# Kernel optimization log

Measured on AMD Instinct MI355X. Metric: run time of the kernel, lower is better.

## Reference

```python
import jax, jax.numpy as jnp
import numpy as np

N_NODES = 50000
N_EDGES = 800000
D_IN = 512
D_HID = 256


def gcn_conv(x, W, b, src, dst, n_nodes):
    """PyG-style GCNConv: self-loops + symmetric normalization.
    x: [N, d_in], W: [d_in, d_out], b: [d_out], src/dst: [E] (already include self-loops? no -> add here)
    """
    loops = jnp.arange(n_nodes, dtype=src.dtype)
    src_f = jnp.concatenate([src, loops])  # [E+N]
    dst_f = jnp.concatenate([dst, loops])
    deg = jax.ops.segment_sum(jnp.ones_like(dst_f, dtype=x.dtype), dst_f,
                              num_segments=n_nodes)  # [N]
    dinv = jnp.where(deg > 0, jax.lax.rsqrt(deg), 0.0)
    norm = dinv[src_f] * dinv[dst_f]  # [E+N]
    h = x @ W  # [N, d_out] -- dense GEMM
    msg = h[src_f] * norm[:, None]  # gather + scale, [E+N, d_out]
    out = jax.ops.segment_sum(msg, dst_f, num_segments=n_nodes)  # scatter-add
    return out + b


def setup_inputs() -> dict:
    key = jax.random.key(0)
    k1, k2, k3, k4, k5 = jax.random.split(key, 5)
    x = jax.random.normal(k1, (N_NODES, D_IN), dtype=jnp.float32)
    edge_index = jax.random.randint(k2, (2, N_EDGES), 0, N_NODES, dtype=jnp.int32)
    # Glorot-ish init for weights
    W1 = jax.random.normal(k3, (D_IN, D_HID), dtype=jnp.float32) / np.sqrt(D_IN)
    W2 = jax.random.normal(k4, (D_HID, D_HID), dtype=jnp.float32) / np.sqrt(D_HID)
    b1 = jnp.zeros((D_HID,), dtype=jnp.float32)
    b2 = jnp.zeros((D_HID,), dtype=jnp.float32)
    return {"x": x, "edge_index": edge_index, "W1": W1, "b1": b1, "W2": W2, "b2": b2}


def reference(x, edge_index, W1, b1, W2, b2):
    n_nodes = x.shape[0]
    src, dst = edge_index[0], edge_index[1]
    h = jax.nn.relu(gcn_conv(x, W1, b1, src, dst, n_nodes))
    h = gcn_conv(h, W2, b2, src, dst, n_nodes)
    # edge-level gather-dot scoring
    score = jnp.einsum('ed,ed->e', h[src], h[dst])  # [E]
    prob_edge = jax.nn.sigmoid(score)
    return prob_edge
```

## Files before the change

### kernel.cpp

```cpp
#include <hip/hip_runtime.h>
#include <stdint.h>

#define D_IN 512
#define D_HID 256

typedef __attribute__((ext_vector_type(8))) short bf16x8;
typedef __attribute__((ext_vector_type(8))) unsigned short u16x8;
typedef __attribute__((ext_vector_type(4))) float f32x4;

__device__ __forceinline__ float b2f(unsigned short u) {
    union { float f; uint32_t i; } x; x.i = ((uint32_t)u) << 16; return x.f;
}
__device__ __forceinline__ unsigned short f2b(float f) {
    union { float f; uint32_t i; } x; x.f = f;
    uint32_t i = x.i;
    uint32_t r = (i + 0x7FFFu + ((i >> 16) & 1u)) >> 16;
    return (unsigned short)r;
}

__device__ __forceinline__ void async_copy16(const unsigned short* g, unsigned short* lds) {
    __builtin_amdgcn_global_load_lds((const __attribute__((address_space(1))) unsigned int*)g,
                                     (__attribute__((address_space(3))) unsigned int*)lds,
                                     16, 0, 0);
}

__global__ __launch_bounds__(256) void detect_dtype_kernel(const ushort4* __restrict__ raw,
                                                           int n4, int* __restrict__ flag) {
    int i = blockIdx.x * blockDim.x + threadIdx.x;
    int hit = 0;
    if (i < n4) {
        ushort4 u = raw[i];
        hit = ((((u.x >> 7) & 0xFF) == 0xFF) || (((u.y >> 7) & 0xFF) == 0xFF) ||
               (((u.z >> 7) & 0xFF) == 0xFF) || (((u.w >> 7) & 0xFF) == 0xFF)) ? 1 : 0;
    }
    unsigned long long b = __ballot(hit);
    if ((threadIdx.x & 63) == 0 && b != 0ULL) atomicOr(flag, 1);
}

__device__ __forceinline__ void wpack_body(const void* __restrict__ W,
        unsigned short* __restrict__ Wp, int K, bool f32, int t) {
    int total = (K >> 6) * 2 * 16 * 64;
    if (t >= total) return;
    int lane = t & 63;
    int c = (t >> 6) & 15;
    int h = (t >> 10) & 1;
    int kk = t >> 11;
    int n = c * 16 + (lane & 15);
    int k0 = kk * 64 + h * 32 + (lane >> 4) * 8;
    u16x8 o;
#pragma unroll
    for (int j = 0; j < 8; ++j) {
        float v = f32 ? ((const float*)W)[(size_t)(k0 + j) * 256 + n]
                      : b2f(((const unsigned short*)W)[(size_t)(k0 + j) * 256 + n]);
        o[j] = f2b(v);
    }
    *(u16x8*)(Wp + (size_t)t * 8) = o;
}

__global__ __launch_bounds__(256) void pre_fused_kernel(const int* __restrict__ dst,
        int* __restrict__ counts, int E,
        const void* __restrict__ W1, unsigned short* __restrict__ Wp1,
        const void* __restrict__ W2, unsigned short* __restrict__ Wp2,
        const int* __restrict__ flag, int histBlocks, int wp1Blocks) {
    int b = blockIdx.x;
    if (b < histBlocks) {
        int e = b * 256 + threadIdx.x;
        if (e < E) atomicAdd(&counts[dst[e]], 1);
        return;
    }
    b -= histBlocks;
    bool f32 = (*flag != 0);
    if (b < wp1Blocks) {
        wpack_body(W1, Wp1, D_IN, f32, b * 256 + threadIdx.x);
    } else {
        wpack_body(W2, Wp2, D_HID, f32, (b - wp1Blocks) * 256 + threadIdx.x);
    }
}

__global__ __launch_bounds__(256) void partial_sum_kernel(const int* __restrict__ counts,
        int* __restrict__ partial, int n) {
    __shared__ int sh[4];
    int b = blockIdx.x;
    int lane = threadIdx.x & 63, wv = threadIdx.x >> 6;
    int s = 0;
    for (int j = threadIdx.x; j < 1024; j += 256) {
        int i = b * 1024 + j;
        s += (i < n) ? counts[i] : 0;
    }
#pragma unroll
    for (int off = 32; off > 0; off >>= 1) s += __shfl_down(s, off, 64);
    if (lane == 0) sh[wv] = s;
    __syncthreads();
    if (threadIdx.x == 0) partial[b] = sh[0] + sh[1] + sh[2] + sh[3];
}

__global__ void scan_partials_kernel(int* __restrict__ partial, int nb,
                                     int* __restrict__ indptr, int N) {
    int lane = threadIdx.x & 63;
    int orig = (lane < nb) ? partial[lane] : 0;
    int v = orig;
#pragma unroll
    for (int off = 1; off < 64; off <<= 1) {
        int u = __shfl(v, lane - off, 64);
        if (lane >= off) v += u;
    }
    int tot = __shfl(v, nb - 1, 64);
    if (lane < nb) partial[lane] = v - orig;
    if (lane == 0) indptr[N] = tot;
}

__global__ __launch_bounds__(1024) void scan_chunk_kernel(const int* __restrict__ counts,
        const int* __restrict__ partial, int* __restrict__ indptr, int* __restrict__ cursor,
        float* __restrict__ dinv, int n) {
    __shared__ int sh[1024];
    int b = blockIdx.x;
    int i = b * 1024 + threadIdx.x;
    int v = (i < n) ? counts[i] : 0;
    sh[threadIdx.x] = v;
    __syncthreads();
    for (int off = 1; off < 1024; off <<= 1) {
        int t = (threadIdx.x >= off) ? sh[threadIdx.x - off] : 0;
        __syncthreads();
        sh[threadIdx.x] += t;
        __syncthreads();
    }
    if (i < n) {
        int e = partial[b] + sh[threadIdx.x] - v;
        indptr[i] = e;
        cursor[i] = e;
        dinv[i] = rsqrtf((float)(v + 1));
    }
}

template<int K, bool MF32, bool FUSE>
__global__ __launch_bounds__(256) void gemm_bf16(const void* __restrict__ Ain,
        const unsigned short* __restrict__ Wp, unsigned short* __restrict__ C, int M,
        const int* __restrict__ flag,
        const int* __restrict__ eidx, int* __restrict__ cursor, int* __restrict__ csr_src,
        int* __restrict__ csr_dst, int* __restrict__ pos_of, int E, int sblocks) {
    __shared__ unsigned short As[2][64 * 64];
    constexpr int NK = K / 64;
    int bid = blockIdx.x;
    if (FUSE) {
        if (bid < sblocks) {
            int e = bid * 256 + (int)threadIdx.x;
            if (e < E) {
                int d = eidx[(size_t)E + e];
                int pos = atomicAdd(&cursor[d], 1);
                csr_src[pos] = eidx[e];
                csr_dst[pos] = d;
                pos_of[e] = pos;
            }
            return;
        }
        bid -= sblocks;
    }
    int t = threadIdx.x;
    int lane = t & 63, wv = t >> 6;
    int n0 = lane & 15, grp = lane >> 4;
    int row0 = bid * 64;

    int srow = wv * 16 + (lane >> 3);
    int segp = lane & 7;

    f32x4 acc[4][4];
#pragma unroll
    for (int rt = 0; rt < 4; ++rt)
#pragma unroll
        for (int ct = 0; ct < 4; ++ct) acc[rt][ct] = (f32x4){0.f, 0.f, 0.f, 0.f};

    auto compute_tile = [&](int kk, const unsigned short* Abuf) {
        bf16x8 bw[4][2];
#pragma unroll
        for (int ct = 0; ct < 4; ++ct)
#pragma unroll
            for (int h = 0; h < 2; ++h)
                bw[ct][h] = *(const bf16x8*)(Wp +
                    ((size_t)(((kk * 2 + h) * 16) + (wv * 4 + ct)) * 64 + lane) * 8);
#pragma unroll
        for (int rt = 0; rt < 4; ++rt) {
            int r = rt * 16 + n0;
#pragma unroll
            for (int h = 0; h < 2; ++h) {
                int sp = (h * 4 + grp + r) & 7;
                bf16x8 a = *(const bf16x8*)(Abuf + r * 64 + sp * 8);
#pragma unroll
                for (int ct = 0; ct < 4; ++ct)
                    acc[rt][ct] = __builtin_amdgcn_mfma_f32_16x16x32_bf16(a, bw[ct][h],
                                                                          acc[rt][ct], 0, 0, 0);
            }
        }
    };

    bool f32src = MF32 && (*flag != 0);
    if (f32src) {
        const float* A = (const float*)Ain;
        auto stage_f32 = [&](int buf, const float4* pr) {
#pragma unroll
            for (int j = 0; j < 2; ++j) {
                u16x8 o;
#pragma unroll
                for (int q = 0; q < 4; ++q) {
                    o[q]     = f2b(pr[j * 2 + 0][q]);
                    o[q + 4] = f2b(pr[j * 2 + 1][q]);
                }
                *(u16x8*)(&As[buf][0] + wv * 1024 + j * 512 + lane * 8) = o;
            }
        };
        auto load_f32 = [&](int kof, float4* pr) {
#pragma unroll
            for (int j = 0; j < 2; ++j) {
                int row = srow + j * 8;
                int s = (segp - row) & 7;
                const float* g = A + (size_t)min(row0 + row, M - 1) * K + kof + s * 8;
                pr[j * 2 + 0] = *(const float4*)(g);
                pr[j * 2 + 1] = *(const float4*)(g + 4);
            }
        };
        float4 pr[4];
        load_f32(0, pr);
        stage_f32(0, pr);
        for (int kk = 0; kk < NK; ++kk) {
            int cur = kk & 1;
            if (kk + 1 < NK) load_f32((kk + 1) * 64, pr);
            asm volatile("s_waitcnt lgkmcnt(0)" ::: "memory");
            __builtin_amdgcn_s_barrier();
            compute_tile(kk, &As[cur][0]);
            if (kk + 1 < NK) stage_f32(cur ^ 1, pr);
        }
    } else {
        const unsigned short* A = (const unsigned short*)Ain;
#pragma unroll
        for (int j = 0; j < 2; ++j) {
            int row = srow + j * 8;
            int s = (segp - row) & 7;
            const unsigned short* g = A + (size_t)min(row0 + row, M - 1) * K + s * 8;
            async_copy16(g, &As[0][0] + wv * 1024 + j * 512);
        }
        asm volatile("s_waitcnt vmcnt(0)" ::: "memory");
        __builtin_amdgcn_s_barrier();
        for (int kk = 0; kk < NK; ++kk) {
            int cur = kk & 1;
            if (kk + 1 < NK) {
                int kof = (kk + 1) * 64;
#pragma unroll
                for (int j = 0; j < 2; ++j) {
                    int row = srow + j * 8;
                    int s = (segp - row) & 7;
                    const unsigned short* g = A + (size_t)min(row0 + row, M - 1) * K + kof + s * 8;
                    async_copy16(g, &As[cur ^ 1][0] + wv * 1024 + j * 512);
                }
            }
            compute_tile(kk, &As[cur][0]);
            asm volatile("s_waitcnt vmcnt(0)" ::: "memory");
            __builtin_amdgcn_s_barrier();
        }
    }
#pragma unroll
    for (int rt = 0; rt < 4; ++rt) {
#pragma unroll
        for (int ct = 0; ct < 4; ++ct) {
#pragma unroll
            for (int reg = 0; reg < 4; ++reg) {
                int row = row0 + rt * 16 + grp * 4 + reg;
                if (row < M)
                    C[(size_t)row * 256 + (wv * 4 + ct) * 16 + n0] = f2b(acc[rt][ct][reg]);
            }
        }
    }
}

__global__ __launch_bounds__(256) void aggregate_kernel(const unsigned short* __restrict__ h,
        const int* __restrict__ indptr, const int* __restrict__ csr_src,
        const float* __restrict__ dinv, const void* __restrict__ bias,
        unsigned short* __restrict__ out, int n, int do_relu, const int* __restrict__ flag) {
    int wave = threadIdx.x >> 6;
    int lane = threadIdx.x & 63;
    int half = lane >> 5;
    int hl = lane & 31;
    int v = blockIdx.x * 4 + wave;
    if (v >= n) return;
    int beg = indptr[v];
    int end = indptr[v + 1];
    float dv = dinv[v];

    float acc[8];
    if (half == 0) {
        u16x8 hv = *(const u16x8*)(h + (size_t)v * 256 + hl * 8);
#pragma unroll
        for (int i = 0; i < 8; ++i) acc[i] = dv * b2f(hv[i]);
    } else {
#pragma unroll
        for (int i = 0; i < 8; ++i) acc[i] = 0.f;
    }

    float wA = 0.f, wB = 0.f, wC = 0.f;
    u16x8 rA = (u16x8)0, rB = (u16x8)0, rC = (u16x8)0;
    auto ld = [&](int idx, float& w, u16x8& r) {
        if (idx < end) {
            int s = csr_src[idx];
            w = dinv[s];
            r = *(const u16x8*)(h + (size_t)s * 256 + hl * 8);
        } else {
            w = 0.f;
        }
    };
    int e = beg + half;
    ld(e, wA, rA);
    ld(e + 2, wB, rB);
    ld(e + 4, wC, rC);
    while (e + 4 < end) {
#pragma unroll
        for (int i = 0; i < 8; ++i) acc[i] += wA * b2f(rA[i]);
        ld(e + 6, wA, rA);
#pragma unroll
        for (int i = 0; i < 8; ++i) acc[i] += wB * b2f(rB[i]);
        ld(e + 8, wB, rB);
#pragma unroll
        for (int i = 0; i < 8; ++i) acc[i] += wC * b2f(rC[i]);
        ld(e + 10, wC, rC);
        e += 6;
    }
#pragma unroll
    for (int i = 0; i < 8; ++i)
        acc[i] += wA * b2f(rA[i]) + wB * b2f(rB[i]) + wC * b2f(rC[i]);

#pragma unroll
    for (int i = 0; i < 8; ++i) acc[i] += __shfl_xor(acc[i], 32, 64);

    if (half == 0) {
        float bb[8];
        if (*flag != 0) {
            const float* bp = (const float*)bias + hl * 8;
#pragma unroll
            for (int i = 0; i < 8; ++i) bb[i] = bp[i];
        } else {
            const unsigned short* bp = (const unsigned short*)bias + hl * 8;
#pragma unroll
            for (int i = 0; i < 8; ++i) bb[i] = b2f(bp[i]);
        }
        u16x8 ov;
#pragma unroll
        for (int i = 0; i < 8; ++i) {
            float o = dv * acc[i] + bb[i];
            if (do_relu) o = fmaxf(o, 0.f);
            ov[i] = f2b(o);
        }
        *(u16x8*)(out + (size_t)v * 256 + hl * 8) = ov;
    }
}

__global__ __launch_bounds__(256) void edge_score_mfma(const unsigned short* __restrict__ h,
        const int* __restrict__ csr_src, const int* __restrict__ csr_dst,
        float* __restrict__ tmp, int E) {
    int lane = threadIdx.x & 63;
    int wv = threadIdx.x >> 6;
    int base = (blockIdx.x * 4 + wv) * 16;
    if (base >= E) return;
    int m = lane & 15, grp = lane >> 4;
    int e = base + m;
    int ec = min(e, E - 1);
    int s = csr_src[ec], d = csr_dst[ec];
    const unsigned short* hs = h + (size_t)s * 256 + grp * 8;
    const unsigned short* hd = h + (size_t)d * 256 + grp * 8;
    f32x4 acc = {0.f, 0.f, 0.f, 0.f};
#pragma unroll
    for (int kk = 0; kk < 8; ++kk) {
        bf16x8 a = *(const bf16x8*)(hs + kk * 32);
        bf16x8 b = *(const bf16x8*)(hd + kk * 32);
        acc = __builtin_amdgcn_mfma_f32_16x16x32_bf16(a, b, acc, 0, 0, 0);
    }
    int reg = m - grp * 4;
    if (reg >= 0 && reg < 4 && e < E) {
        float p = (reg == 0) ? acc[0] : (reg == 1) ? acc[1] : (reg == 2) ? acc[2] : acc[3];
        tmp[e] = 1.f / (1.f + __expf(-p));
    }
}

__global__ __launch_bounds__(256) void permute_out_kernel(const float* __restrict__ tmp,
        const int* __restrict__ pos_of, void* __restrict__ out, int E,
        const int* __restrict__ flag) {
    int e = blockIdx.x * blockDim.x + threadIdx.x;
    if (e >= E) return;
    float p = tmp[pos_of[e]];
    if (*flag != 0)
        ((float*)out)[e] = p;
    else
        ((unsigned short*)out)[e] = f2b(p);
}

extern "C" void kernel_launch(void* const* d_in, const int* in_sizes, int n_in,
                              void* d_out, int out_size, void* d_ws, size_t ws_size,
                              hipStream_t stream) {
    const void* x  = d_in[0];
    const int* edge_index = (const int*)d_in[1];
    const void* W1 = d_in[2];
    const void* b1 = d_in[3];
    const void* W2 = d_in[4];
    const void* b2 = d_in[5];

    const int N = in_sizes[0] / D_IN;
    const int E = in_sizes[1] / 2;
    const int* dst = edge_index + E;

    char* ws = (char*)d_ws;
    size_t off = 0;
    auto alloc = [&](size_t bytes) {
        char* p = ws + off;
        off = (off + bytes + 255) & ~(size_t)255;
        return p;
    };
    int* flag     = (int*)alloc(256);
    float* dinv   = (float*)alloc((size_t)N * 4);
    int* counts   = (int*)alloc((size_t)N * 4);
    int* indptr   = (int*)alloc((size_t)(N + 1) * 4);
    int* cursor   = (int*)alloc((size_t)N * 4);
    int* partial  = (int*)alloc(64 * 4);
    int* csr_src  = (int*)alloc((size_t)E * 4);
    int* csr_dst  = (int*)alloc((size_t)E * 4);
    int* pos_of   = (int*)alloc((size_t)E * 4);
    float* ptmp   = (float*)alloc((size_t)E * 4);
    unsigned short* Wp1 = (unsigned short*)alloc((size_t)D_IN * 256 * 2);
    unsigned short* Wp2 = (unsigned short*)alloc((size_t)D_HID * 256 * 2);
    unsigned short* hA  = (unsigned short*)alloc((size_t)N * 256 * 2);
    unsigned short* hB  = (unsigned short*)alloc((size_t)N * 256 * 2);

    const int nb = (N + 1023) / 1024;
    const int sblocks = (E + 255) / 256;
    const int wp1Blocks = (D_IN * 32) / 256;
    const int wp2Blocks = (D_HID * 32) / 256;
    const int ggrid = (N + 63) / 64;

    hipMemsetAsync(flag, 0, 4, stream);
    hipMemsetAsync(counts, 0, (size_t)N * 4, stream);
    detect_dtype_kernel<<<64, 256, 0, stream>>>((const ushort4*)x, 16384, flag);
    pre_fused_kernel<<<sblocks + wp1Blocks + wp2Blocks, 256, 0, stream>>>(
        dst, counts, E, W1, Wp1, W2, Wp2, flag, sblocks, wp1Blocks);
    partial_sum_kernel<<<nb, 256, 0, stream>>>(counts, partial, N);
    scan_partials_kernel<<<1, 64, 0, stream>>>(partial, nb, indptr, N);
    scan_chunk_kernel<<<nb, 1024, 0, stream>>>(counts, partial, indptr, cursor, dinv, N);

    gemm_bf16<D_IN, true, true><<<sblocks + ggrid, 256, 0, stream>>>(
        x, Wp1, hA, N, flag, edge_index, cursor, csr_src, csr_dst, pos_of, E, sblocks);
    aggregate_kernel<<<(N + 3) / 4, 256, 0, stream>>>(hA, indptr, csr_src, dinv, b1, hB, N, 1, flag);
    gemm_bf16<D_HID, false, false><<<ggrid, 256, 0, stream>>>(
        hB, Wp2, hA, N, flag, nullptr, nullptr, nullptr, nullptr, nullptr, 0, 0);
    aggregate_kernel<<<(N + 3) / 4, 256, 0, stream>>>(hA, indptr, csr_src, dinv, b2, hB, N, 0, flag);
    edge_score_mfma<<<(E + 63) / 64, 256, 0, stream>>>(hB, csr_src, csr_dst, ptmp, E);
    permute_out_kernel<<<(E + 255) / 256, 256, 0, stream>>>(ptmp, pos_of, d_out, E, flag);
}
```

Before: 476.7 us.

## Fuse layer-1 aggregation with layer-2 GEMM and write csr_dst from indptr

Adds agg_gemm_kernel, which aggregates 64 rows of neighbour features (with bias and ReLU) into LDS and then multiplies them by W2 with MFMA in the same block. This removes the round trip of the intermediate hidden tensor through global memory and one kernel launch. The fused GEMM grid also reorders its blocks so GEMM blocks come first, and csr_dst is filled per node from indptr instead of by scattered per-edge writes. The risk is that the aggregation phase now runs with only one block per 64 rows, which gives less latency hiding. The LDS footprint is also larger.

```diff
diff --git a/kernel.cpp b/kernel.cpp
--- a/kernel.cpp
+++ b/kernel.cpp
@@ -137,23 +137,32 @@
         const unsigned short* __restrict__ Wp, unsigned short* __restrict__ C, int M,
         const int* __restrict__ flag,
         const int* __restrict__ eidx, int* __restrict__ cursor, int* __restrict__ csr_src,
-        int* __restrict__ csr_dst, int* __restrict__ pos_of, int E, int sblocks) {
+        int* __restrict__ csr_dst, int* __restrict__ pos_of,
+        const int* __restrict__ indptr, int E, int sblocks) {
     __shared__ unsigned short As[2][64 * 64];
     constexpr int NK = K / 64;
     int bid = blockIdx.x;
+    int gblocks = (M + 63) >> 6;
     if (FUSE) {
-        if (bid < sblocks) {
-            int e = bid * 256 + (int)threadIdx.x;
-            if (e < E) {
-                int d = eidx[(size_t)E + e];
-                int pos = atomicAdd(&cursor[d], 1);
-                csr_src[pos] = eidx[e];
-                csr_dst[pos] = d;
-                pos_of[e] = pos;
+        if (bid >= gblocks) {
+            int tb = bid - gblocks;
+            if (tb < sblocks) {
+                int e = tb * 256 + (int)threadIdx.x;
+                if (e < E) {
+                    int d = eidx[(size_t)E + e];
+                    int pos = atomicAdd(&cursor[d], 1);
+                    csr_src[pos] = eidx[e];
+                    pos_of[e] = pos;
+                }
+            } else {
+                int v = (tb - sblocks) * 256 + (int)threadIdx.x;
+                if (v < M) {
+                    int b0 = indptr[v], e0 = indptr[v + 1];
+                    for (int p = b0; p < e0; ++p) csr_dst[p] = v;
+                }
             }
             return;
         }
-        bid -= sblocks;
     }
     int t = threadIdx.x;
     int lane = t & 63, wv = t >> 6;
@@ -265,6 +274,135 @@
                 int row = row0 + rt * 16 + grp * 4 + reg;
                 if (row < M)
                     C[(size_t)row * 256 + (wv * 4 + ct) * 16 + n0] = f2b(acc[rt][ct][reg]);
+            }
+        }
+    }
+}
+
+__global__ __launch_bounds__(256) void agg_gemm_kernel(const unsigned short* __restrict__ h,
+        const int* __restrict__ indptr, const int* __restrict__ csr_src,
+        const float* __restrict__ dinv, const void* __restrict__ bias,
+        const unsigned short* __restrict__ Wp, unsigned short* __restrict__ C,
+        int n, const int* __restrict__ flag) {
+    __shared__ unsigned short T[4][64 * 64];
+    int t = threadIdx.x;
+    int lane = t & 63, wv = t >> 6;
+    int half = lane >> 5, hl = lane & 31;
+    int row0 = blockIdx.x * 64;
+
+    float bb[8];
+    if (*flag != 0) {
+        const float* bp = (const float*)bias + hl * 8;
+#pragma unroll
+        for (int i = 0; i < 8; ++i) bb[i] = bp[i];
+    } else {
+        const unsigned short* bp = (const unsigned short*)bias + hl * 8;
+#pragma unroll
+        for (int i = 0; i < 8; ++i) bb[i] = b2f(bp[i]);
+    }
+
+    for (int i = 0; i < 16; ++i) {
+        int r = wv * 16 + i;
+        int v = row0 + r;
+        int kk = hl >> 3, s = hl & 7, sp = (s + r) & 7;
+        if (v < n) {
+            int beg = indptr[v];
+            int end = indptr[v + 1];
+            float dv = dinv[v];
+            float acc[8];
+            if (half == 0) {
+                u16x8 hv = *(const u16x8*)(h + (size_t)v * 256 + hl * 8);
+#pragma unroll
+                for (int j = 0; j < 8; ++j) acc[j] = dv * b2f(hv[j]);
+            } else {
+#pragma unroll
+                for (int j = 0; j < 8; ++j) acc[j] = 0.f;
+            }
+            float wA = 0.f, wB = 0.f, wC = 0.f;
+            u16x8 rA = (u16x8)0, rB = (u16x8)0, rC = (u16x8)0;
+            auto ld = [&](int idx, float& w, u16x8& r2) {
+                if (idx < end) {
+                    int s2 = csr_src[idx];
+                    w = dinv[s2];
+                    r2 = *(const u16x8*)(h + (size_t)s2 * 256 + hl * 8);
+                } else {
+                    w = 0.f;
+                }
+            };
+            int e = beg + half;
+            ld(e, wA, rA);
+            ld(e + 2, wB, rB);
+            ld(e + 4, wC, rC);
+            while (e + 4 < end) {
+#pragma unroll
+                for (int j = 0; j < 8; ++j) acc[j] += wA * b2f(rA[j]);
+                ld(e + 6, wA, rA);
+#pragma unroll
+                for (int j = 0; j < 8; ++j) acc[j] += wB * b2f(rB[j]);
+                ld(e + 8, wB, rB);
+#pragma unroll
+                for (int j = 0; j < 8; ++j) acc[j] += wC * b2f(rC[j]);
+                ld(e + 10, wC, rC);
+                e += 6;
+            }
+#pragma unroll
+            for (int j = 0; j < 8; ++j)
+                acc[j] += wA * b2f(rA[j]) + wB * b2f(rB[j]) + wC * b2f(rC[j]);
+#pragma unroll
+            for (int j = 0; j < 8; ++j) acc[j] += __shfl_xor(acc[j], 32, 64);
+            if (half == 0) {
+                u16x8 o;
+#pragma unroll
+                for (int j = 0; j < 8; ++j) {
+                    float ov = fmaxf(dv * acc[j] + bb[j], 0.f);
+                    o[j] = f2b(ov);
+                }
+                *(u16x8*)(&T[kk][0] + r * 64 + sp * 8) = o;
+            }
+        } else if (half == 0) {
+            *(u16x8*)(&T[kk][0] + r * 64 + sp * 8) = (u16x8)0;
+        }
+    }
+    __syncthreads();
+
+    int n0 = lane & 15, grp = lane >> 4;
+    f32x4 acc2[4][4];
+#pragma unroll
+    for (int rt = 0; rt < 4; ++rt)
+#pragma unroll
+        for (int ct = 0; ct < 4; ++ct) acc2[rt][ct] = (f32x4){0.f, 0.f, 0.f, 0.f};
+#pragma unroll
+    for (int kk = 0; kk < 4; ++kk) {
+        bf16x8 bw[4][2];
+#pragma unroll
+        for (int ct = 0; ct < 4; ++ct)
+#pragma unroll
+            for (int h2 = 0; h2 < 2; ++h2)
+                bw[ct][h2] = *(const bf16x8*)(Wp +
+                    ((size_t)(((kk * 2 + h2) * 16) + (wv * 4 + ct)) * 64 + lane) * 8);
+#pragma unroll
+        for (int rt = 0; rt < 4; ++rt) {
+            int r = rt * 16 + n0;
+#pragma unroll
+            for (int h2 = 0; h2 < 2; ++h2) {
+                int sp = (h2 * 4 + grp + r) & 7;
+                bf16x8 a = *(const bf16x8*)(&T[kk][0] + r * 64 + sp * 8);
+#pragma unroll
+                for (int ct = 0; ct < 4; ++ct)
+                    acc2[rt][ct] = __builtin_amdgcn_mfma_f32_16x16x32_bf16(a, bw[ct][h2],
+                                                                           acc2[rt][ct], 0, 0, 0);
+            }
+        }
+    }
+#pragma unroll
+    for (int rt = 0; rt < 4; ++rt) {
+#pragma unroll
+        for (int ct = 0; ct < 4; ++ct) {
+#pragma unroll
+            for (int reg = 0; reg < 4; ++reg) {
+                int row = row0 + rt * 16 + grp * 4 + reg;
+                if (row < n)
+                    C[(size_t)row * 256 + (wv * 4 + ct) * 16 + n0] = f2b(acc2[rt][ct][reg]);
             }
         }
     }
@@ -427,6 +565,7 @@
 
     const int nb = (N + 1023) / 1024;
     const int sblocks = (E + 255) / 256;
+    const int fblocks = (N + 255) / 256;
     const int wp1Blocks = (D_IN * 32) / 256;
     const int wp2Blocks = (D_HID * 32) / 256;
     const int ggrid = (N + 63) / 64;
@@ -440,12 +579,10 @@
     scan_partials_kernel<<<1, 64, 0, stream>>>(partial, nb, indptr, N);
     scan_chunk_kernel<<<nb, 1024, 0, stream>>>(counts, partial, indptr, cursor, dinv, N);
 
-    gemm_bf16<D_IN, true, true><<<sblocks + ggrid, 256, 0, stream>>>(
-        x, Wp1, hA, N, flag, edge_index, cursor, csr_src, csr_dst, pos_of, E, sblocks);
-    aggregate_kernel<<<(N + 3) / 4, 256, 0, stream>>>(hA, indptr, csr_src, dinv, b1, hB, N, 1, flag);
-    gemm_bf16<D_HID, false, false><<<ggrid, 256, 0, stream>>>(
-        hB, Wp2, hA, N, flag, nullptr, nullptr, nullptr, nullptr, nullptr, 0, 0);
-    aggregate_kernel<<<(N + 3) / 4, 256, 0, stream>>>(hA, indptr, csr_src, dinv, b2, hB, N, 0, flag);
-    edge_score_mfma<<<(E + 63) / 64, 256, 0, stream>>>(hB, csr_src, csr_dst, ptmp, E);
+    gemm_bf16<D_IN, true, true><<<ggrid + sblocks + fblocks, 256, 0, stream>>>(
+        x, Wp1, hA, N, flag, edge_index, cursor, csr_src, csr_dst, pos_of, indptr, E, sblocks);
+    agg_gemm_kernel<<<ggrid, 256, 0, stream>>>(hA, indptr, csr_src, dinv, b1, Wp2, hB, N, flag);
+    aggregate_kernel<<<(N + 3) / 4, 256, 0, stream>>>(hB, indptr, csr_src, dinv, b2, hA, N, 0, flag);
+    edge_score_mfma<<<(E + 63) / 64, 256, 0, stream>>>(hA, csr_src, csr_dst, ptmp, E);
     permute_out_kernel<<<(E + 255) / 256, 256, 0, stream>>>(ptmp, pos_of, d_out, E, flag);
 }
```

Result: slower. 538.1 us (+12.9%).
